# Kernel optimization log

Hardware: AMD Instinct MI355X
Metric: run time of the kernel (lower is better)

## Reference

```python
import jax, jax.numpy as jnp
import numpy as np

N_MOL, P_PRO, HID, HEADS, B = 2048, 2048, 64, 16, 64


def setup_inputs() -> dict:
    key = jax.random.key(0)
    ks = jax.random.split(key, 9)
    s = 0.1  # weight scale
    return {
        "mol_feats": jax.random.normal(ks[0], (N_MOL, HID), jnp.float32),
        "fused_feats": jax.random.normal(ks[1], (P_PRO, HID), jnp.float32),
        "Wmu": jax.random.normal(ks[2], (2 * HID, HEADS), jnp.float32) * s,
        "bmu": jax.random.normal(ks[3], (HEADS,), jnp.float32) * s,
        "W1": jax.random.normal(ks[4], (HEADS, 2 * HEADS), jnp.float32) * s,
        "b1": jax.random.normal(ks[5], (2 * HEADS,), jnp.float32) * s,
        "W2": jax.random.normal(ks[6], (2 * HEADS, 1), jnp.float32) * s,
        "b2": jax.random.normal(ks[7], (1,), jnp.float32) * s,
        "mol_batch": jnp.sort(jax.random.randint(ks[8], (N_MOL,), 0, B)).astype(jnp.int64),
        "num_graphs": B,
    }


def reference(mol_feats, fused_feats, Wmu, bmu, W1, b1, W2, b2, mol_batch, num_graphs):
    H = mol_feats.shape[1]
    # In the torch code: atom_pairs = cat([mol_feats[mol_index], fused_feats[pro_index]])
    # with mol_index/pro_index forming the full ligand-atom x protein-atom cross product.
    # Split the Linear weight so cat+gather becomes a broadcast sum (same math).
    a_mol = mol_feats @ Wmu[:H] + bmu          # [N, heads]
    a_pro = fused_feats @ Wmu[H:]              # [P, heads]
    mu = jax.nn.elu(a_mol[:, None, :] + a_pro[None, :, :]) + 1.0  # [N, P, heads]
    # scatter_sum over mol_index == sum over all protein atoms per ligand atom
    y_atom = jnp.sum(mu, axis=1)               # [N, heads]
    # scatter_sum over mol_batch: atom -> graph
    y = jax.ops.segment_sum(y_atom, mol_batch, num_segments=num_graphs) * 0.001  # [B, heads]
    y = jax.nn.elu(y @ W1 + b1)
    return y @ W2 + b2                          # [B, 1]
```

## Files before the change

### kernel.cpp

```cpp
#include <hip/hip_runtime.h>

#define N_MOL 2048
#define P_PRO 2048
#define HID   64
#define HEADS 16
#define NGRAPH 64

#define OFF_EAMOL 32768
#define OFF_APRO  65536
#define OFF_YSUM  131072

__global__ __launch_bounds__(256) void k1_proj(
    const float* __restrict__ mol, const float* __restrict__ pro,
    const float* __restrict__ Wmu, const float* __restrict__ bmu,
    float* __restrict__ ws)
{
    __shared__ float fs[16 * 64];
    __shared__ float wsh[64 * 16];
    const int tid = threadIdx.x;
    const int blk = blockIdx.x;

    if (blk == 0) {
        float4 z; z.x = z.y = z.z = z.w = 0.0f;
        ((float4*)(ws + OFF_YSUM))[tid] = z;
    }

    const bool isMol = blk < (N_MOL / 16);
    const int rowbase = (isMol ? blk : blk - (N_MOL / 16)) * 16;
    const float* feats = isMol ? (mol + rowbase * HID) : (pro + rowbase * HID);
    const float* wsrc  = Wmu + (isMol ? 0 : HID * HEADS);

    ((float4*)fs)[tid]  = ((const float4*)feats)[tid];
    ((float4*)wsh)[tid] = ((const float4*)wsrc)[tid];
    __syncthreads();

    const int h = tid & 15, r = tid >> 4;
    float acc = isMol ? bmu[h] : 0.0f;
#pragma unroll
    for (int k = 0; k < 64; ++k)
        acc += fs[r * 64 + k] * wsh[k * 16 + h];

    float* a_out = ws + (isMol ? 0 : OFF_APRO);
    float* e_out = a_out + 32768;
    const int idx = (rowbase + r) * 16 + h;
    a_out[idx] = acc;
    e_out[idx] = __expf(acc);
}

__global__ __launch_bounds__(256) void k2_pair(
    const float* __restrict__ ws_in, const int* __restrict__ batch,
    float* __restrict__ ysum)
{
    const float* a_mol  = ws_in;
    const float* ea_mol = ws_in + OFF_EAMOL;
    const float* a_pro  = ws_in + OFF_APRO;
    const float* ea_pro = ws_in + OFF_APRO + 32768;

    const int tid = threadIdx.x;
    const int h = tid & 15, g = tid >> 4;
    const int nt = blockIdx.x >> 2, pt = blockIdx.x & 3;
    const int nbase = nt * 8;
    const int pflat = pt * (512 * 16);

    float a1[8], ea[8], acc[8];
#pragma unroll
    for (int j = 0; j < 8; ++j) {
        const int idx = (nbase + j) * 16 + h;
        a1[j]  = a_mol[idx] + 1.0f;
        ea[j]  = ea_mol[idx];
        acc[j] = 0.0f;
    }

#pragma unroll 4
    for (int i = 0; i < 32; ++i) {
        const int flat = pflat + i * 256 + tid;
        const float bp = a_pro[flat];
        const float eb = ea_pro[flat];
#pragma unroll
        for (int j = 0; j < 8; ++j) {
            const float s1 = a1[j] + bp;
            const float e  = ea[j] * eb;
            acc[j] += (s1 > 1.0f) ? s1 : e;
        }
    }

    __shared__ float red[8 * 16 * 16];
#pragma unroll
    for (int j = 0; j < 8; ++j)
        red[j * 256 + g * 16 + h] = acc[j];
    __syncthreads();
    if (tid < 128) {
        const int j = tid >> 4, hh = tid & 15;
        float s = 0.0f;
#pragma unroll
        for (int g2 = 0; g2 < 16; ++g2)
            s += red[j * 256 + g2 * 16 + hh];
        const int b = batch[nbase + j];
        atomicAdd(&ysum[b * 16 + hh], s);
    }
}

__global__ __launch_bounds__(64) void k3_final(
    const float* __restrict__ ysum,
    const float* __restrict__ W1, const float* __restrict__ b1,
    const float* __restrict__ W2, const float* __restrict__ b2,
    float* __restrict__ out)
{
    const int b = threadIdx.x;
    float yv[HEADS];
#pragma unroll
    for (int hh = 0; hh < HEADS; ++hh) yv[hh] = ysum[b * 16 + hh] * 0.001f;
    float o = b2[0];
#pragma unroll
    for (int j = 0; j < 32; ++j) {
        float t = b1[j];
#pragma unroll
        for (int hh = 0; hh < HEADS; ++hh) t += yv[hh] * W1[hh * 32 + j];
        t = (t > 0.0f) ? t : (__expf(t) - 1.0f);
        o += t * W2[j];
    }
    out[b] = o;
}

extern "C" void kernel_launch(void* const* d_in, const int* in_sizes, int n_in,
                              void* d_out, int out_size, void* d_ws, size_t ws_size,
                              hipStream_t stream) {
    const float* mol   = (const float*)d_in[0];
    const float* pro   = (const float*)d_in[1];
    const float* Wmu   = (const float*)d_in[2];
    const float* bmu   = (const float*)d_in[3];
    const float* W1    = (const float*)d_in[4];
    const float* b1    = (const float*)d_in[5];
    const float* W2    = (const float*)d_in[6];
    const float* b2    = (const float*)d_in[7];
    const int*   batch = (const int*)d_in[8];
    float* ws = (float*)d_ws;

    hipLaunchKernelGGL(k1_proj, dim3(256), dim3(256), 0, stream,
                       mol, pro, Wmu, bmu, ws);
    hipLaunchKernelGGL(k2_pair, dim3(1024), dim3(256), 0, stream,
                       ws, batch, ws + OFF_YSUM);
    hipLaunchKernelGGL(k3_final, dim3(1), dim3(64), 0, stream,
                       ws + OFF_YSUM, W1, b1, W2, b2, (float*)d_out);
}
```

Before: 103.8 us.

## Replace global atomics with per-tile partials and a segmented reduction in the final kernel

The pair kernel now writes per-atom partial sums for each of its four protein tiles into a workspace buffer, instead of doing atomicAdd into per-graph accumulators. The final kernel runs one block per graph. Each block finds its contiguous segment in the sorted batch array, sums the partials for that segment, and applies the MLP with a wavefront shuffle reduction. Projections and their exponentials are also stored interleaved as float2, so each element needs one vector load. This removes heavy atomic contention and the zero-init step, but it relies on the batch array being sorted and adds an extra pass over the partial buffer.

```diff
diff --git a/kernel.cpp b/kernel.cpp
--- a/kernel.cpp
+++ b/kernel.cpp
@@ -6,9 +6,8 @@
 #define HEADS 16
 #define NGRAPH 64
 
-#define OFF_EAMOL 32768
-#define OFF_APRO  65536
-#define OFF_YSUM  131072
+#define OFF_PEPRO 65536
+#define OFF_YPART 131072
 
 __global__ __launch_bounds__(256) void k1_proj(
     const float* __restrict__ mol, const float* __restrict__ pro,
@@ -19,12 +18,6 @@
     __shared__ float wsh[64 * 16];
     const int tid = threadIdx.x;
     const int blk = blockIdx.x;
-
-    if (blk == 0) {
-        float4 z; z.x = z.y = z.z = z.w = 0.0f;
-        ((float4*)(ws + OFF_YSUM))[tid] = z;
-    }
-
     const bool isMol = blk < (N_MOL / 16);
     const int rowbase = (isMol ? blk : blk - (N_MOL / 16)) * 16;
     const float* feats = isMol ? (mol + rowbase * HID) : (pro + rowbase * HID);
@@ -40,21 +33,17 @@
     for (int k = 0; k < 64; ++k)
         acc += fs[r * 64 + k] * wsh[k * 16 + h];
 
-    float* a_out = ws + (isMol ? 0 : OFF_APRO);
-    float* e_out = a_out + 32768;
+    float2* pe = (float2*)(ws + (isMol ? 0 : OFF_PEPRO));
     const int idx = (rowbase + r) * 16 + h;
-    a_out[idx] = acc;
-    e_out[idx] = __expf(acc);
+    float2 v; v.x = acc; v.y = __expf(acc);
+    pe[idx] = v;
 }
 
 __global__ __launch_bounds__(256) void k2_pair(
-    const float* __restrict__ ws_in, const int* __restrict__ batch,
-    float* __restrict__ ysum)
+    const float* __restrict__ ws_in, float* __restrict__ y_part)
 {
-    const float* a_mol  = ws_in;
-    const float* ea_mol = ws_in + OFF_EAMOL;
-    const float* a_pro  = ws_in + OFF_APRO;
-    const float* ea_pro = ws_in + OFF_APRO + 32768;
+    const float2* pe_mol = (const float2*)ws_in;
+    const float2* pe_pro = (const float2*)(ws_in + OFF_PEPRO);
 
     const int tid = threadIdx.x;
     const int h = tid & 15, g = tid >> 4;
@@ -65,17 +54,16 @@
     float a1[8], ea[8], acc[8];
 #pragma unroll
     for (int j = 0; j < 8; ++j) {
-        const int idx = (nbase + j) * 16 + h;
-        a1[j]  = a_mol[idx] + 1.0f;
-        ea[j]  = ea_mol[idx];
+        const float2 m = pe_mol[(nbase + j) * 16 + h];
+        a1[j]  = m.x + 1.0f;
+        ea[j]  = m.y;
         acc[j] = 0.0f;
     }
 
 #pragma unroll 4
     for (int i = 0; i < 32; ++i) {
-        const int flat = pflat + i * 256 + tid;
-        const float bp = a_pro[flat];
-        const float eb = ea_pro[flat];
+        const float2 p = pe_pro[pflat + i * 256 + tid];
+        const float bp = p.x, eb = p.y;
 #pragma unroll
         for (int j = 0; j < 8; ++j) {
             const float s1 = a1[j] + bp;
@@ -95,31 +83,61 @@
 #pragma unroll
         for (int g2 = 0; g2 < 16; ++g2)
             s += red[j * 256 + g2 * 16 + hh];
-        const int b = batch[nbase + j];
-        atomicAdd(&ysum[b * 16 + hh], s);
+        y_part[pt * 32768 + (nbase + j) * 16 + hh] = s;
     }
 }
 
-__global__ __launch_bounds__(64) void k3_final(
-    const float* __restrict__ ysum,
+__global__ __launch_bounds__(256) void k3_seg_mlp(
+    const float* __restrict__ y_part, const int* __restrict__ batch,
     const float* __restrict__ W1, const float* __restrict__ b1,
     const float* __restrict__ W2, const float* __restrict__ b2,
     float* __restrict__ out)
 {
-    const int b = threadIdx.x;
-    float yv[HEADS];
+    const int tid = threadIdx.x;
+    const int b = blockIdx.x;
+    __shared__ int s_start, s_end;
+    if (tid == 0) { s_start = 0; s_end = 0; }
+    __syncthreads();
+
+    for (int i = tid; i < N_MOL; i += 256) {
+        const int bi = batch[i];
+        if (bi == b) {
+            if (i == 0 || batch[i - 1] != b) s_start = i;
+            if (i == N_MOL - 1 || batch[i + 1] != b) s_end = i + 1;
+        }
+    }
+    __syncthreads();
+
+    const int h = tid & 15, rr = tid >> 4;
+    float s = 0.0f;
+    for (int n = s_start + rr; n < s_end; n += 16) {
+        const int o = n * 16 + h;
+        s += y_part[o] + y_part[32768 + o] + y_part[65536 + o] + y_part[98304 + o];
+    }
+
+    __shared__ float red[256];
+    __shared__ float ysum[HEADS];
+    red[tid] = s;
+    __syncthreads();
+    if (tid < 16) {
+        float c = 0.0f;
 #pragma unroll
-    for (int hh = 0; hh < HEADS; ++hh) yv[hh] = ysum[b * 16 + hh] * 0.001f;
-    float o = b2[0];
-#pragma unroll
-    for (int j = 0; j < 32; ++j) {
+        for (int r2 = 0; r2 < 16; ++r2) c += red[r2 * 16 + tid];
+        ysum[tid] = c * 0.001f;
+    }
+    __syncthreads();
+
+    if (tid < 32) {
+        const int j = tid;
         float t = b1[j];
 #pragma unroll
-        for (int hh = 0; hh < HEADS; ++hh) t += yv[hh] * W1[hh * 32 + j];
+        for (int hh = 0; hh < HEADS; ++hh) t += ysum[hh] * W1[hh * 32 + j];
         t = (t > 0.0f) ? t : (__expf(t) - 1.0f);
-        o += t * W2[j];
+        float v = t * W2[j];
+#pragma unroll
+        for (int off = 16; off > 0; off >>= 1) v += __shfl_down(v, off, 32);
+        if (tid == 0) out[b] = v + b2[0];
     }
-    out[b] = o;
 }
 
 extern "C" void kernel_launch(void* const* d_in, const int* in_sizes, int n_in,
@@ -139,7 +157,7 @@
     hipLaunchKernelGGL(k1_proj, dim3(256), dim3(256), 0, stream,
                        mol, pro, Wmu, bmu, ws);
     hipLaunchKernelGGL(k2_pair, dim3(1024), dim3(256), 0, stream,
-                       ws, batch, ws + OFF_YSUM);
-    hipLaunchKernelGGL(k3_final, dim3(1), dim3(64), 0, stream,
-                       ws + OFF_YSUM, W1, b1, W2, b2, (float*)d_out);
+                       ws, ws + OFF_YPART);
+    hipLaunchKernelGGL(k3_seg_mlp, dim3(NGRAPH), dim3(256), 0, stream,
+                       ws + OFF_YPART, batch, W1, b1, W2, b2, (float*)d_out);
 }
```

Result: faster. 86.86 us (-16.3%).
